# Kernel optimization log

Measured on AMD Instinct MI355X. Metric: run time of the kernel, lower is better.

Reference implementation:

```python
import jax, jax.numpy as jnp
import numpy as np

S, B, H, V, T = 128, 64, 512, 100, 32  # src_len, batch, hidden, vocab, tgt_len


def setup_inputs() -> dict:
    key = jax.random.key(0)
    ks = jax.random.split(key, 12)
    sc = 0.05
    return {
        "encoder_outputs": jax.random.normal(ks[0], (S, B, H), jnp.float32),
        "W_emb": jax.random.normal(ks[1], (V, H), jnp.float32) * sc,   # embedding.weight.T (Linear(V->H, no bias) on one-hot)
        "W_comb": jax.random.normal(ks[2], (H, 2 * H), jnp.float32) * sc,
        "b_comb": jnp.zeros((H,), jnp.float32),
        "W_ih": jax.random.normal(ks[3], (3 * H, H), jnp.float32) * sc,
        "W_hh": jax.random.normal(ks[4], (3 * H, H), jnp.float32) * sc,
        "b_ih": jnp.zeros((3 * H,), jnp.float32),
        "b_hh": jnp.zeros((3 * H,), jnp.float32),
        "W_out": jax.random.normal(ks[5], (V, H), jnp.float32) * sc,
        "b_out": jnp.zeros((V,), jnp.float32),
        "w_vat": jax.random.normal(ks[6], (H,), jnp.float32) * sc,     # vat: Linear(H->1)
        "b_vat": jnp.zeros((), jnp.float32),
        "target_seq": jax.random.randint(ks[7], (T, B), 0, V),
    }


def reference(encoder_outputs, W_emb, W_comb, b_comb, W_ih, W_hh, b_ih, b_hh,
              W_out, b_out, w_vat, b_vat, target_seq):
    # train_forward with teacher forcing, dropout in eval (identity).
    def step(h, sym):  # h: [B,H], sym: [B] int
        embedded = W_emb[sym]                                   # one-hot @ embedding.weight.T
        # Bahdanau additive attention: scores over src positions
        scores = jnp.tanh(encoder_outputs + h[None]) @ w_vat + b_vat   # [S,B]
        attn = jax.nn.softmax(scores, axis=0)                   # softmax over S
        ctx = jnp.einsum('sb,sbh->bh', attn, encoder_outputs)   # [B,H]
        x = jax.nn.relu(jnp.concatenate([embedded, ctx], axis=-1) @ W_comb.T + b_comb)
        # PyTorch GRU cell
        gi = x @ W_ih.T + b_ih                                   # [B,3H]
        gh = h @ W_hh.T + b_hh
        ir, iz, inn = jnp.split(gi, 3, axis=-1)
        hr, hz, hn = jnp.split(gh, 3, axis=-1)
        r = jax.nn.sigmoid(ir + hr)
        z = jax.nn.sigmoid(iz + hz)
        n = jnp.tanh(inn + r * hn)
        h_new = (1.0 - z) * n + z * h
        logits = jax.nn.log_softmax(h_new @ W_out.T + b_out, axis=-1)  # [B,V]
        return h_new, logits

    h0 = jnp.zeros((encoder_outputs.shape[1], W_hh.shape[1]), encoder_outputs.dtype)
    _, logits = jax.lax.scan(step, h0, target_seq[:-1])          # [T-1,B,V]
    return jnp.transpose(logits, (1, 0, 2))                      # [B,T-1,V]
```

## Files before the change

### kernel.cpp

```cpp
#include <hip/hip_runtime.h>
#include <hip/hip_fp16.h>

#define Sn 128
#define Bn 64
#define Hn 512
#define Vn 100
#define TSn 31

typedef unsigned int   u32;
typedef unsigned short u16;
typedef _Float16 f16x2 __attribute__((ext_vector_type(2)));
typedef _Float16 f16x8 __attribute__((ext_vector_type(8)));
typedef float    f32x4 __attribute__((ext_vector_type(4)));

#define OFF_ENC2  0ull
#define OFF_WC2M  8388608ull
#define OFF_WIHM  8912896ull
#define OFF_WHHM  10485760ull
#define OFF_WOUTM 12058624ull
#define OFF_EMB2  12173312ull
#define OFF_GB    12378112ull

#define NT_IH 1536
#define NT_HH 1536
#define NT_C2 512
#define NT_OUT 112

__device__ __forceinline__ u16 f2h(float f){ _Float16 h=(_Float16)f; return __builtin_bit_cast(u16,h); }
__device__ __forceinline__ f16x2 uh2(u32 u){ return __builtin_bit_cast(f16x2,u); }
__device__ __forceinline__ float2 h2f(u32 u){ f16x2 h=uh2(u); return make_float2((float)h.x,(float)h.y); }
__device__ __forceinline__ u32 pack2h(float a, float b){ return (u32)f2h(a) | ((u32)f2h(b) << 16); }

__device__ __forceinline__ float fast_tanh(float x){
    float e = __expf(2.0f*x);
    return 1.0f - 2.0f/(e + 1.0f);
}
__device__ __forceinline__ float fast_sigmoid(float x){ return 1.0f/(1.0f + __expf(-x)); }

__device__ __forceinline__ float wave_sum(float v){
#pragma unroll
    for (int o = 32; o; o >>= 1) v += __shfl_xor(v, o);
    return v;
}
__device__ __forceinline__ float wave_max(float v){
#pragma unroll
    for (int o = 32; o; o >>= 1) v = fmaxf(v, __shfl_xor(v, o));
    return v;
}

__device__ __forceinline__ f32x4 mfma16(f16x8 a, f16x8 b, f32x4 c){
    return __builtin_amdgcn_mfma_f32_16x16x32_f16(a, b, c, 0, 0, 0);
}
__device__ __forceinline__ f16x8 ldB(const uint4* base, int tile, int lane){
    return __builtin_bit_cast(f16x8, base[(size_t)tile*64 + lane]);
}
__device__ __forceinline__ f16x8 ldA(const u32* v32, int kf, int lane){
    return __builtin_bit_cast(f16x8, ((const uint4*)v32)[kf*4 + (lane>>4)]);
}

__global__ __launch_bounds__(256) void prep_enc(
    const float* __restrict__ enc, const float* __restrict__ bih,
    const float* __restrict__ bhh, char* __restrict__ ws)
{
    const int t0 = blockIdx.x*256 + threadIdx.x;
    const int stride = gridDim.x*256;
    u16* de = (u16*)(ws + OFF_ENC2);
    for (int c = t0; c < Sn*Bn*Hn/4; c += stride) {
        const int h4 = c & 127;
        const int s  = (c >> 7) & 127;
        const int bb = c >> 14;
        float4 v = ((const float4*)enc)[(s*Bn + bb)*(Hn/4) + h4];
        ushort4 o;
        o.x = f2h(v.x); o.y = f2h(v.y); o.z = f2h(v.z); o.w = f2h(v.w);
        ((ushort4*)de)[c] = o;
    }
    float* GB = (float*)(ws + OFF_GB);
    for (int j = t0; j < Hn; j += stride) {
        GB[j]        = bih[j]        + bhh[j];
        GB[Hn + j]   = bih[Hn + j]   + bhh[Hn + j];
        GB[2*Hn + j] = bih[2*Hn + j];
        GB[3*Hn + j] = bhh[2*Hn + j];
    }
}

__global__ __launch_bounds__(256) void prep_pack(
    const float* __restrict__ Wih, const float* __restrict__ Whh,
    const float* __restrict__ Wcomb, const float* __restrict__ Wout,
    char* __restrict__ ws)
{
    const int total = (NT_IH + NT_HH + NT_C2 + NT_OUT)*64;
    for (int id = blockIdx.x*256 + threadIdx.x; id < total; id += gridDim.x*256) {
        const int l = id & 63;
        const int tile = id >> 6;
        const int kofs = ((l >> 4)*8);
        const float* s = nullptr;
        uint4* dst = nullptr;
        if (tile < NT_IH) {
            const int g = tile >> 9, jt = (tile >> 4) & 31, kf = tile & 15;
            s = Wih + ((size_t)(g*Hn + jt*16 + (l & 15)))*Hn + kf*32 + kofs;
            dst = (uint4*)(ws + OFF_WIHM) + (size_t)tile*64 + l;
        } else if (tile < NT_IH + NT_HH) {
            const int tt = tile - NT_IH;
            const int g = tt >> 9, jt = (tt >> 4) & 31, kf = tt & 15;
            s = Whh + ((size_t)(g*Hn + jt*16 + (l & 15)))*Hn + kf*32 + kofs;
            dst = (uint4*)(ws + OFF_WHHM) + (size_t)tt*64 + l;
        } else if (tile < NT_IH + NT_HH + NT_C2) {
            const int tt = tile - NT_IH - NT_HH;
            const int jt = tt >> 4, kf = tt & 15;
            s = Wcomb + ((size_t)(jt*16 + (l & 15)))*(2*Hn) + Hn + kf*32 + kofs;
            dst = (uint4*)(ws + OFF_WC2M) + (size_t)tt*64 + l;
        } else {
            const int tt = tile - NT_IH - NT_HH - NT_C2;
            const int jt = tt >> 4, kf = tt & 15;
            const int v = jt*16 + (l & 15);
            dst = (uint4*)(ws + OFF_WOUTM) + (size_t)tt*64 + l;
            if (v < Vn) s = Wout + (size_t)v*Hn + kf*32 + kofs;
        }
        uint4 val = {0u,0u,0u,0u};
        if (s) {
            const float4 a = *(const float4*)s;
            const float4 c = *(const float4*)(s + 4);
            val.x = pack2h(a.x, a.y); val.y = pack2h(a.z, a.w);
            val.z = pack2h(c.x, c.y); val.w = pack2h(c.z, c.w);
        }
        *dst = val;
    }
}

__global__ __launch_bounds__(512) void prep_emb2(
    const float* __restrict__ Wemb, const float* __restrict__ Wcomb,
    const float* __restrict__ bcomb, char* __restrict__ ws)
{
    float* EMB2 = (float*)(ws + OFF_EMB2);
    const int w = threadIdx.x >> 6;
    const int lane = threadIdx.x & 63;
    const int j = blockIdx.x*8 + w;
    const float4* wc = (const float4*)(Wcomb + (size_t)j*2*Hn);
    const float bc = bcomb[j];
#pragma unroll
    for (int pass = 0; pass < 2; ++pass) {
        const int v = lane + 64*pass;
        if (v < Vn) {
            const float4* we = (const float4*)(Wemb + (size_t)v*Hn);
            float acc = 0.0f;
            for (int k4 = 0; k4 < 128; ++k4) {
                const float4 a = wc[k4], b = we[k4];
                acc += a.x*b.x + a.y*b.y + a.z*b.z + a.w*b.w;
            }
            EMB2[(size_t)v*Hn + j] = acc + bc;
        }
    }
}

__global__ __launch_bounds__(1024) void bahdanau_decoder(
    const float* __restrict__ bout, const float* __restrict__ wvat,
    const float* __restrict__ bvat, const int* __restrict__ tgt,
    float* __restrict__ out, const char* __restrict__ ws)
{
    const uint4* WC2M  = (const uint4*)(ws + OFF_WC2M);
    const uint4* WIHM  = (const uint4*)(ws + OFF_WIHM);
    const uint4* WHHM  = (const uint4*)(ws + OFF_WHHM);
    const uint4* WOUTM = (const uint4*)(ws + OFF_WOUTM);
    const float* EMB2  = (const float*)(ws + OFF_EMB2);
    const float* GB    = (const float*)(ws + OFF_GB);

    extern __shared__ __align__(16) u16 enc_lds[];
    __shared__ __align__(16) float h_full[Hn];
    __shared__ __align__(16) u16   hn16[Hn];
    __shared__ __align__(16) u16   x16[Hn];
    __shared__ __align__(16) u32   ctx32[Hn/2];
    __shared__ __align__(16) float scores_s[Sn];
    __shared__ __align__(16) float attnw_s[Sn];
    __shared__ __align__(16) float ghacc[3][Hn];
    __shared__ __align__(16) float llog[128];

    const int tid  = threadIdx.x;
    const int lane = tid & 63;
    const int wid  = tid >> 6;
    const int b    = blockIdx.x;

    {
        const uint4* src = (const uint4*)(ws + OFF_ENC2 + (size_t)b*Sn*Hn*2);
        for (int i = tid; i < Sn*Hn/8; i += 1024) ((uint4*)enc_lds)[i] = src[i];
    }
    if (tid < Hn) { h_full[tid] = 0.0f; hn16[tid] = 0; }
    const float4 Wa = ((const float4*)wvat)[2*lane];
    const float4 Wb = ((const float4*)wvat)[2*lane+1];
    const float bv = bvat[0];
    __syncthreads();

    for (int t = 0; t < TSn; ++t) {
        if (wid < 4) {
            const float4 Ha = ((const float4*)h_full)[2*lane];
            const float4 Hb = ((const float4*)h_full)[2*lane+1];
            for (int i = 0; i < 32; ++i) {
                const int s = wid + 4*i;
                const uint4 E = ((const uint4*)(enc_lds + s*Hn))[lane];
                const float2 e0 = h2f(E.x), e1 = h2f(E.y), e2 = h2f(E.z), e3 = h2f(E.w);
                float acc = fast_tanh(e0.x+Ha.x)*Wa.x + fast_tanh(e0.y+Ha.y)*Wa.y
                          + fast_tanh(e1.x+Ha.z)*Wa.z + fast_tanh(e1.y+Ha.w)*Wa.w
                          + fast_tanh(e2.x+Hb.x)*Wb.x + fast_tanh(e2.y+Hb.y)*Wb.y
                          + fast_tanh(e3.x+Hb.z)*Wb.z + fast_tanh(e3.y+Hb.w)*Wb.w;
                acc = wave_sum(acc);
                if (lane == 0) scores_s[s] = acc + bv;
            }
        } else if (wid < 15) {
#pragma unroll
            for (int i = 0; i < 4; ++i) {
                const int tt = (wid - 4) + 11*i;
                if (tt < 96) {
                    f32x4 acc = {0.f,0.f,0.f,0.f};
#pragma unroll 4
                    for (int kf = 0; kf < 16; ++kf)
                        acc = mfma16(ldA((const u32*)hn16, kf, lane),
                                     ldB(WHHM, tt*16 + kf, lane), acc);
                    if (lane < 16) ghacc[tt >> 5][(tt & 31)*16 + lane] = acc[0];
                }
            }
        } else {
#pragma unroll
            for (int tt = 0; tt < 7; ++tt) {
                f32x4 acc = {0.f,0.f,0.f,0.f};
#pragma unroll 4
                for (int kf = 0; kf < 16; ++kf)
                    acc = mfma16(ldA((const u32*)hn16, kf, lane),
                                 ldB(WOUTM, tt*16 + kf, lane), acc);
                if (lane < 16) {
                    const int v = tt*16 + lane;
                    if (v < Vn) llog[v] = acc[0] + bout[v];
                }
            }
            if (t > 0) {
                const float l0 = llog[lane];
                const float l1 = (lane < 36) ? llog[64+lane] : -3.0e38f;
                const float mx = wave_max(fmaxf(l0, l1));
                const float e0 = __expf(l0 - mx);
                const float e1 = (lane < 36) ? __expf(l1 - mx) : 0.0f;
                const float lse = mx + __logf(wave_sum(e0 + e1));
                float* op = out + ((size_t)b*TSn + (t-1))*Vn;
                op[lane] = l0 - lse;
                if (lane < 36) op[64 + lane] = l1 - lse;
            }
        }
        __syncthreads();

        if (wid == 0) {
            const float s0 = scores_s[lane], s1 = scores_s[lane+64];
            const float mx = wave_max(fmaxf(s0, s1));
            const float e0 = __expf(s0-mx), e1 = __expf(s1-mx);
            const float inv = 1.0f / wave_sum(e0 + e1);
            attnw_s[lane]    = e0 * inv;
            attnw_s[lane+64] = e1 * inv;
        } else if (wid >= 4 && wid < 15) {
#pragma unroll
            for (int i = 4; i < 7; ++i) {
                const int tt = (wid - 4) + 11*i;
                if (tt < 96) {
                    f32x4 acc = {0.f,0.f,0.f,0.f};
#pragma unroll 4
                    for (int kf = 0; kf < 16; ++kf)
                        acc = mfma16(ldA((const u32*)hn16, kf, lane),
                                     ldB(WHHM, tt*16 + kf, lane), acc);
                    if (lane < 16) ghacc[tt >> 5][(tt & 31)*16 + lane] = acc[0];
                }
            }
        }
        __syncthreads();

        if (wid < 4) {
            const int op = tid;
            float ax = 0.0f, ay = 0.0f;
#pragma unroll 8
            for (int s = 0; s < Sn; ++s) {
                const float a = attnw_s[s];
                const float2 ef = h2f(((const u32*)enc_lds)[s*256 + op]);
                ax += a*ef.x; ay += a*ef.y;
            }
            ctx32[op] = pack2h(ax, ay);
        } else if (wid < 15) {
#pragma unroll
            for (int i = 7; i < 9; ++i) {
                const int tt = (wid - 4) + 11*i;
                if (tt < 96) {
                    f32x4 acc = {0.f,0.f,0.f,0.f};
#pragma unroll 4
                    for (int kf = 0; kf < 16; ++kf)
                        acc = mfma16(ldA((const u32*)hn16, kf, lane),
                                     ldB(WHHM, tt*16 + kf, lane), acc);
                    if (lane < 16) ghacc[tt >> 5][(tt & 31)*16 + lane] = acc[0];
                }
            }
        }
        __syncthreads();

        {
            const int sym = tgt[t*Bn + b];
#pragma unroll
            for (int rep = 0; rep < 2; ++rep) {
                const int jt = wid + rep*16;
                f32x4 acc = {0.f,0.f,0.f,0.f};
#pragma unroll 4
                for (int kf = 0; kf < 16; ++kf)
                    acc = mfma16(ldA(ctx32, kf, lane), ldB(WC2M, jt*16 + kf, lane), acc);
                if (lane < 16) {
                    const int j = jt*16 + lane;
                    const float xv = acc[0] + EMB2[(size_t)sym*Hn + j];
                    x16[j] = f2h(fmaxf(xv, 0.0f));
                }
            }
        }
        __syncthreads();

#pragma unroll
        for (int rep = 0; rep < 2; ++rep) {
            const int jt = wid + rep*16;
            f32x4 aR = {0.f,0.f,0.f,0.f}, aZ = {0.f,0.f,0.f,0.f}, aNi = {0.f,0.f,0.f,0.f};
#pragma unroll 4
            for (int kf = 0; kf < 16; ++kf) {
                const f16x8 ax = ldA((const u32*)x16, kf, lane);
                aR  = mfma16(ax, ldB(WIHM, (0*32 + jt)*16 + kf, lane), aR);
                aZ  = mfma16(ax, ldB(WIHM, (1*32 + jt)*16 + kf, lane), aZ);
                aNi = mfma16(ax, ldB(WIHM, (2*32 + jt)*16 + kf, lane), aNi);
            }
            if (lane < 16) {
                const int j = jt*16 + lane;
                const float r = fast_sigmoid(aR[0]  + ghacc[0][j] + GB[j]);
                const float z = fast_sigmoid(aZ[0]  + ghacc[1][j] + GB[Hn + j]);
                const float n = fast_tanh(aNi[0] + GB[2*Hn + j] + r*(ghacc[2][j] + GB[3*Hn + j]));
                const float hv = (1.0f - z)*n + z*h_full[j];
                h_full[j] = hv;
                hn16[j] = f2h(hv);
            }
        }
        __syncthreads();
    }

    if (wid == 15) {
#pragma unroll
        for (int tt = 0; tt < 7; ++tt) {
            f32x4 acc = {0.f,0.f,0.f,0.f};
#pragma unroll 4
            for (int kf = 0; kf < 16; ++kf)
                acc = mfma16(ldA((const u32*)hn16, kf, lane),
                             ldB(WOUTM, tt*16 + kf, lane), acc);
            if (lane < 16) {
                const int v = tt*16 + lane;
                if (v < Vn) llog[v] = acc[0] + bout[v];
            }
        }
        const float l0 = llog[lane];
        const float l1 = (lane < 36) ? llog[64+lane] : -3.0e38f;
        const float mx = wave_max(fmaxf(l0, l1));
        const float e0 = __expf(l0 - mx);
        const float e1 = (lane < 36) ? __expf(l1 - mx) : 0.0f;
        const float lse = mx + __logf(wave_sum(e0 + e1));
        float* op = out + ((size_t)b*TSn + (TSn-1))*Vn;
        op[lane] = l0 - lse;
        if (lane < 36) op[64 + lane] = l1 - lse;
    }
}

extern "C" void kernel_launch(void* const* d_in, const int* in_sizes, int n_in,
                              void* d_out, int out_size, void* d_ws, size_t ws_size,
                              hipStream_t stream) {
    const float* enc   = (const float*)d_in[0];
    const float* Wemb  = (const float*)d_in[1];
    const float* Wcomb = (const float*)d_in[2];
    const float* bcomb = (const float*)d_in[3];
    const float* Wih   = (const float*)d_in[4];
    const float* Whh   = (const float*)d_in[5];
    const float* bih   = (const float*)d_in[6];
    const float* bhh   = (const float*)d_in[7];
    const float* Wout  = (const float*)d_in[8];
    const float* bout  = (const float*)d_in[9];
    const float* wvat  = (const float*)d_in[10];
    const float* bvat  = (const float*)d_in[11];
    const int*   tgt   = (const int*)d_in[12];
    float* out = (float*)d_out;
    char*  ws  = (char*)d_ws;

    prep_enc<<<512, 256, 0, stream>>>(enc, bih, bhh, ws);
    prep_pack<<<512, 256, 0, stream>>>(Wih, Whh, Wcomb, Wout, ws);
    prep_emb2<<<64, 512, 0, stream>>>(Wemb, Wcomb, bcomb, ws);

    bahdanau_decoder<<<dim3(Bn), dim3(1024), (size_t)(Sn*Hn*2), stream>>>(
        bout, wvat, bvat, tgt, out, ws);
}
```

Measured before the change: 1.324 ms.

## Split each batch row across four cooperative blocks with split-K GEMV partials

The decoder now launches 256 cooperative blocks instead of 64, with four sibling blocks per batch element, placed on the same XCD group. Each block computes a quarter of the K dimension for the W_hh and W_ih GEMVs and a quarter of the combine output. Partial sums go to global scratch and are exchanged through a per-batch atomic counter barrier, after which every block reduces them and runs the GRU update redundantly. The context reduction is also spread across all 16 waves. The aim is to use more CUs and cut per-block MFMA and weight-load latency on the serial recurrence, at the cost of a global-memory barrier and partial-sum round trip every timestep, plus redundant attention work in each sibling.

```diff
diff --git a/kernel.cpp b/kernel.cpp
--- a/kernel.cpp
+++ b/kernel.cpp
@@ -1,5 +1,6 @@
 #include <hip/hip_runtime.h>
 #include <hip/hip_fp16.h>
+#include <hip/hip_cooperative_groups.h>
 
 #define Sn 128
 #define Bn 64
@@ -20,6 +21,8 @@
 #define OFF_WOUTM 12058624ull
 #define OFF_EMB2  12173312ull
 #define OFF_GB    12378112ull
+#define OFF_PEX   12386304ull
+#define OFF_CNT   15532032ull
 
 #define NT_IH 1536
 #define NT_HH 1536
@@ -56,6 +59,22 @@
 }
 __device__ __forceinline__ f16x8 ldA(const u32* v32, int kf, int lane){
     return __builtin_bit_cast(f16x8, ((const uint4*)v32)[kf*4 + (lane>>4)]);
+}
+
+__device__ __forceinline__ void sib_arrive(u32* cnt){
+    asm volatile("s_waitcnt vmcnt(0)" ::: "memory");
+    __syncthreads();
+    if (threadIdx.x == 0)
+        __hip_atomic_fetch_add(cnt, 1u, __ATOMIC_RELAXED, __HIP_MEMORY_SCOPE_AGENT);
+}
+__device__ __forceinline__ void sib_wait(u32* cnt, u32 target){
+    if (threadIdx.x == 0) {
+        u32 v;
+        do { __builtin_amdgcn_s_sleep(2);
+             v = __hip_atomic_load(cnt, __ATOMIC_RELAXED, __HIP_MEMORY_SCOPE_AGENT);
+        } while (v < target);
+    }
+    __syncthreads();
 }
 
 __global__ __launch_bounds__(256) void prep_enc(
@@ -81,6 +100,8 @@
         GB[2*Hn + j] = bih[2*Hn + j];
         GB[3*Hn + j] = bhh[2*Hn + j];
     }
+    u32* cnt = (u32*)(ws + OFF_CNT);
+    for (int i = t0; i < 64*16; i += stride) cnt[i] = 0u;
 }
 
 __global__ __launch_bounds__(256) void prep_pack(
@@ -155,7 +176,7 @@
 __global__ __launch_bounds__(1024) void bahdanau_decoder(
     const float* __restrict__ bout, const float* __restrict__ wvat,
     const float* __restrict__ bvat, const int* __restrict__ tgt,
-    float* __restrict__ out, const char* __restrict__ ws)
+    float* __restrict__ out, char* __restrict__ ws)
 {
     const uint4* WC2M  = (const uint4*)(ws + OFF_WC2M);
     const uint4* WIHM  = (const uint4*)(ws + OFF_WIHM);
@@ -163,21 +184,30 @@
     const uint4* WOUTM = (const uint4*)(ws + OFF_WOUTM);
     const float* EMB2  = (const float*)(ws + OFF_EMB2);
     const float* GB    = (const float*)(ws + OFF_GB);
+    float* PEX = (float*)(ws + OFF_PEX);
+    u32*   CNT = (u32*)(ws + OFF_CNT);
 
     extern __shared__ __align__(16) u16 enc_lds[];
     __shared__ __align__(16) float h_full[Hn];
     __shared__ __align__(16) u16   hn16[Hn];
-    __shared__ __align__(16) u16   x16[Hn];
+    __shared__ __align__(16) u16   xq[128];
     __shared__ __align__(16) u32   ctx32[Hn/2];
     __shared__ __align__(16) float scores_s[Sn];
     __shared__ __align__(16) float attnw_s[Sn];
-    __shared__ __align__(16) float ghacc[3][Hn];
+    __shared__ __align__(16) float2 pctx_s[4][256];
+    __shared__ __align__(16) float sumR[Hn], sumZ[Hn], sumNh[Hn], sumNi[Hn];
     __shared__ __align__(16) float llog[128];
 
     const int tid  = threadIdx.x;
     const int lane = tid & 63;
     const int wid  = tid >> 6;
-    const int b    = blockIdx.x;
+    const int bid  = blockIdx.x;
+    const int xcd  = bid & 7;
+    const int lb   = bid >> 3;
+    const int q    = xcd & 3;
+    const int b    = 2*lb + (xcd >> 2);
+    u32* cnt = CNT + b*16;
+    const size_t pbase = ((size_t)b*4 + q)*3072;
 
     {
         const uint4* src = (const uint4*)(ws + OFF_ENC2 + (size_t)b*Sn*Hn*2);
@@ -205,32 +235,35 @@
                 if (lane == 0) scores_s[s] = acc + bv;
             }
         } else if (wid < 15) {
-#pragma unroll
-            for (int i = 0; i < 4; ++i) {
-                const int tt = (wid - 4) + 11*i;
+            const int w = wid - 4;
+#pragma unroll
+            for (int i = 0; i < 9; ++i) {
+                const int tt = w + 11*i;
                 if (tt < 96) {
+                    const int g = tt >> 5, jt = tt & 31;
+                    f32x4 acc = {0.f,0.f,0.f,0.f};
+#pragma unroll
+                    for (int kfl = 0; kfl < 4; ++kfl)
+                        acc = mfma16(ldA((const u32*)hn16, 4*q + kfl, lane),
+                                     ldB(WHHM, (g*32 + jt)*16 + 4*q + kfl, lane), acc);
+                    if (lane < 16)
+                        ((volatile float*)PEX)[pbase + g*512 + jt*16 + lane] = acc[0];
+                }
+            }
+        } else if (q == 0) {
+            if (t > 0) {
+#pragma unroll
+                for (int tt = 0; tt < 7; ++tt) {
                     f32x4 acc = {0.f,0.f,0.f,0.f};
 #pragma unroll 4
                     for (int kf = 0; kf < 16; ++kf)
                         acc = mfma16(ldA((const u32*)hn16, kf, lane),
-                                     ldB(WHHM, tt*16 + kf, lane), acc);
-                    if (lane < 16) ghacc[tt >> 5][(tt & 31)*16 + lane] = acc[0];
+                                     ldB(WOUTM, tt*16 + kf, lane), acc);
+                    if (lane < 16) {
+                        const int v = tt*16 + lane;
+                        if (v < Vn) llog[v] = acc[0] + bout[v];
+                    }
                 }
-            }
-        } else {
-#pragma unroll
-            for (int tt = 0; tt < 7; ++tt) {
-                f32x4 acc = {0.f,0.f,0.f,0.f};
-#pragma unroll 4
-                for (int kf = 0; kf < 16; ++kf)
-                    acc = mfma16(ldA((const u32*)hn16, kf, lane),
-                                 ldB(WOUTM, tt*16 + kf, lane), acc);
-                if (lane < 16) {
-                    const int v = tt*16 + lane;
-                    if (v < Vn) llog[v] = acc[0] + bout[v];
-                }
-            }
-            if (t > 0) {
                 const float l0 = llog[lane];
                 const float l1 = (lane < 36) ? llog[64+lane] : -3.0e38f;
                 const float mx = wave_max(fmaxf(l0, l1));
@@ -251,91 +284,104 @@
             const float inv = 1.0f / wave_sum(e0 + e1);
             attnw_s[lane]    = e0 * inv;
             attnw_s[lane+64] = e1 * inv;
-        } else if (wid >= 4 && wid < 15) {
-#pragma unroll
-            for (int i = 4; i < 7; ++i) {
-                const int tt = (wid - 4) + 11*i;
-                if (tt < 96) {
-                    f32x4 acc = {0.f,0.f,0.f,0.f};
-#pragma unroll 4
-                    for (int kf = 0; kf < 16; ++kf)
-                        acc = mfma16(ldA((const u32*)hn16, kf, lane),
-                                     ldB(WHHM, tt*16 + kf, lane), acc);
-                    if (lane < 16) ghacc[tt >> 5][(tt & 31)*16 + lane] = acc[0];
-                }
-            }
-        }
-        __syncthreads();
-
-        if (wid < 4) {
-            const int op = tid;
+        }
+        __syncthreads();
+
+        {
+            const int op = tid & 255, sc = tid >> 8;
             float ax = 0.0f, ay = 0.0f;
 #pragma unroll 8
-            for (int s = 0; s < Sn; ++s) {
+            for (int i2 = 0; i2 < 32; ++i2) {
+                const int s = sc*32 + i2;
                 const float a = attnw_s[s];
                 const float2 ef = h2f(((const u32*)enc_lds)[s*256 + op]);
                 ax += a*ef.x; ay += a*ef.y;
             }
-            ctx32[op] = pack2h(ax, ay);
-        } else if (wid < 15) {
-#pragma unroll
-            for (int i = 7; i < 9; ++i) {
-                const int tt = (wid - 4) + 11*i;
-                if (tt < 96) {
-                    f32x4 acc = {0.f,0.f,0.f,0.f};
-#pragma unroll 4
-                    for (int kf = 0; kf < 16; ++kf)
-                        acc = mfma16(ldA((const u32*)hn16, kf, lane),
-                                     ldB(WHHM, tt*16 + kf, lane), acc);
-                    if (lane < 16) ghacc[tt >> 5][(tt & 31)*16 + lane] = acc[0];
-                }
-            }
+            pctx_s[sc][op] = make_float2(ax, ay);
+        }
+        __syncthreads();
+        if (tid < 256) {
+            const float2 c0 = pctx_s[0][tid], c1 = pctx_s[1][tid];
+            const float2 c2 = pctx_s[2][tid], c3 = pctx_s[3][tid];
+            ctx32[tid] = pack2h(c0.x+c1.x+c2.x+c3.x, c0.y+c1.y+c2.y+c3.y);
         }
         __syncthreads();
 
         {
             const int sym = tgt[t*Bn + b];
-#pragma unroll
-            for (int rep = 0; rep < 2; ++rep) {
-                const int jt = wid + rep*16;
+            if (wid < 8) {
+                const int jt = 8*q + wid;
                 f32x4 acc = {0.f,0.f,0.f,0.f};
 #pragma unroll 4
                 for (int kf = 0; kf < 16; ++kf)
                     acc = mfma16(ldA(ctx32, kf, lane), ldB(WC2M, jt*16 + kf, lane), acc);
                 if (lane < 16) {
                     const int j = jt*16 + lane;
-                    const float xv = acc[0] + EMB2[(size_t)sym*Hn + j];
-                    x16[j] = f2h(fmaxf(xv, 0.0f));
+                    xq[wid*16 + lane] = f2h(fmaxf(acc[0] + EMB2[(size_t)sym*Hn + j], 0.0f));
                 }
             }
         }
         __syncthreads();
 
 #pragma unroll
-        for (int rep = 0; rep < 2; ++rep) {
-            const int jt = wid + rep*16;
-            f32x4 aR = {0.f,0.f,0.f,0.f}, aZ = {0.f,0.f,0.f,0.f}, aNi = {0.f,0.f,0.f,0.f};
-#pragma unroll 4
-            for (int kf = 0; kf < 16; ++kf) {
-                const f16x8 ax = ldA((const u32*)x16, kf, lane);
-                aR  = mfma16(ax, ldB(WIHM, (0*32 + jt)*16 + kf, lane), aR);
-                aZ  = mfma16(ax, ldB(WIHM, (1*32 + jt)*16 + kf, lane), aZ);
-                aNi = mfma16(ax, ldB(WIHM, (2*32 + jt)*16 + kf, lane), aNi);
-            }
-            if (lane < 16) {
-                const int j = jt*16 + lane;
-                const float r = fast_sigmoid(aR[0]  + ghacc[0][j] + GB[j]);
-                const float z = fast_sigmoid(aZ[0]  + ghacc[1][j] + GB[Hn + j]);
-                const float n = fast_tanh(aNi[0] + GB[2*Hn + j] + r*(ghacc[2][j] + GB[3*Hn + j]));
-                const float hv = (1.0f - z)*n + z*h_full[j];
-                h_full[j] = hv;
-                hn16[j] = f2h(hv);
-            }
-        }
-        __syncthreads();
-    }
-
-    if (wid == 15) {
+        for (int i = 0; i < 6; ++i) {
+            const int tt = wid + 16*i;
+            const int g = tt >> 5, jt = tt & 31;
+            f32x4 acc = {0.f,0.f,0.f,0.f};
+#pragma unroll
+            for (int kfl = 0; kfl < 4; ++kfl)
+                acc = mfma16(ldA((const u32*)xq, kfl, lane),
+                             ldB(WIHM, (g*32 + jt)*16 + 4*q + kfl, lane), acc);
+            if (lane < 16)
+                ((volatile float*)PEX)[pbase + (3 + g)*512 + jt*16 + lane] = acc[0];
+        }
+
+        sib_arrive(cnt);
+        sib_wait(cnt, 4u*(t+1));
+
+        {
+            const volatile float* P = (const volatile float*)PEX + (size_t)b*4*3072;
+            for (int p = tid; p < 2048; p += 1024) {
+                const int kind = p >> 9, j = p & 511;
+                float s = 0.0f;
+                if (kind == 0) {
+#pragma unroll
+                    for (int q2 = 0; q2 < 4; ++q2)
+                        s += P[q2*3072 + j] + P[q2*3072 + 3*512 + j];
+                    sumR[j] = s;
+                } else if (kind == 1) {
+#pragma unroll
+                    for (int q2 = 0; q2 < 4; ++q2)
+                        s += P[q2*3072 + 512 + j] + P[q2*3072 + 4*512 + j];
+                    sumZ[j] = s;
+                } else if (kind == 2) {
+#pragma unroll
+                    for (int q2 = 0; q2 < 4; ++q2)
+                        s += P[q2*3072 + 2*512 + j];
+                    sumNh[j] = s;
+                } else {
+#pragma unroll
+                    for (int q2 = 0; q2 < 4; ++q2)
+                        s += P[q2*3072 + 5*512 + j];
+                    sumNi[j] = s;
+                }
+            }
+        }
+        __syncthreads();
+
+        if (tid < Hn) {
+            const int j = tid;
+            const float r = fast_sigmoid(sumR[j] + GB[j]);
+            const float z = fast_sigmoid(sumZ[j] + GB[Hn + j]);
+            const float n = fast_tanh(sumNi[j] + GB[2*Hn + j] + r*(sumNh[j] + GB[3*Hn + j]));
+            const float hv = (1.0f - z)*n + z*h_full[j];
+            h_full[j] = hv;
+            hn16[j] = f2h(hv);
+        }
+        __syncthreads();
+    }
+
+    if (q == 0 && wid == 15) {
 #pragma unroll
         for (int tt = 0; tt < 7; ++tt) {
             f32x4 acc = {0.f,0.f,0.f,0.f};
@@ -383,6 +429,7 @@
     prep_pack<<<512, 256, 0, stream>>>(Wih, Whh, Wcomb, Wout, ws);
     prep_emb2<<<64, 512, 0, stream>>>(Wemb, Wcomb, bcomb, ws);
 
-    bahdanau_decoder<<<dim3(Bn), dim3(1024), (size_t)(Sn*Hn*2), stream>>>(
-        bout, wvat, bvat, tgt, out, ws);
-}
+    void* args[] = { &bout, &wvat, &bvat, &tgt, &out, &ws };
+    hipLaunchCooperativeKernel((const void*)bahdanau_decoder,
+                               dim3(256), dim3(1024), args, (size_t)(Sn*Hn*2), stream);
+}
```

After: 1.766 ms. 1.33x slower.
